# Kernel tuning notes

Measured on AMD Instinct MI355X. Metric: run time of the kernel, lower is better.

## Reference

```python
import jax, jax.numpy as jnp
import numpy as np

N = 16384   # 32 graphs x 512 nodes
E_RAND = 500000
H, C, D, F, L = 4, 64, 256, 1024, 4  # heads, head_dim, model dim, ffn dim, layers


def setup_inputs() -> dict:
    key = jax.random.key(0)
    ks = jax.random.split(key, 8)
    ei = jax.random.randint(ks[0], (2, E_RAND), 0, N)
    loops = jnp.arange(N)
    edge_index = jnp.concatenate([ei, jnp.stack([loops, loops])], axis=1)  # add_self_loops
    s = 0.05
    return dict(
        hf=jax.random.normal(ks[1], (N, D), dtype=jnp.float32),
        hs=jax.random.normal(ks[2], (N, D), dtype=jnp.float32),
        edge_index=edge_index,
        Wgat=jax.random.normal(ks[3], (2, L, D, D), dtype=jnp.float32) * s,
        att_src=jax.random.normal(ks[4], (2, L, H, C), dtype=jnp.float32) * s,
        att_dst=jax.random.normal(ks[5], (2, L, H, C), dtype=jnp.float32) * s,
        bias_gat=jnp.zeros((2, L, D), dtype=jnp.float32),
        W1=jax.random.normal(ks[6], (2, L, D, F), dtype=jnp.float32) * s,
        b1=jnp.zeros((2, L, F), dtype=jnp.float32),
        W2=jax.random.normal(ks[7], (2, L, F, D), dtype=jnp.float32) * s,
        b2=jnp.zeros((2, L, D), dtype=jnp.float32),
        g1=jnp.ones((2, L, D), dtype=jnp.float32),
        bt1=jnp.zeros((2, L, D), dtype=jnp.float32),
        g2=jnp.ones((2, L, D), dtype=jnp.float32),
        bt2=jnp.zeros((2, L, D), dtype=jnp.float32),
    )


def _ln(x, g, b):
    m = jnp.mean(x, -1, keepdims=True)
    v = jnp.var(x, -1, keepdims=True)
    return (x - m) * jax.lax.rsqrt(v + 1e-5) * g + b


def _gat_encoder_layer(x, src, dst, Wg, asr, ads, bg, W1, b1, W2, b2, g1, bt1, g2, bt2):
    # GATConv (PyG semantics): linear proj, per-edge attention, segment softmax over dst
    h = (x @ Wg).reshape(N, H, C)                       # [N,H,C]
    a_s = (h * asr).sum(-1)                             # [N,H]
    a_d = (h * ads).sum(-1)                             # [N,H]
    e = jax.nn.leaky_relu(a_s[src] + a_d[dst], 0.2)     # [E,H]
    m = jax.ops.segment_max(e, dst, num_segments=N)
    ex = jnp.exp(e - m[dst])
    den = jax.ops.segment_sum(ex, dst, num_segments=N)
    alpha = ex / jnp.maximum(den[dst], 1e-16)           # [E,H]
    agg = jax.ops.segment_sum(h[src] * alpha[:, :, None], dst, num_segments=N)
    out = agg.reshape(N, H * C) + bg                    # concat heads + bias
    # residual + norm1 (dropout=0.0)
    x1 = _ln(out + x, g1, bt1)
    # FFN + residual + norm2
    f = jax.nn.relu(x1 @ W1 + b1) @ W2 + b2
    return _ln(f + x1, g2, bt2)


def reference(hf, hs, edge_index, Wgat, att_src, att_dst, bias_gat, W1, b1, W2, b2, g1, bt1, g2, bt2):
    src, dst = edge_index[0], edge_index[1]
    for i in range(L):
        hf_new = _gat_encoder_layer(hf + hs, src, dst, Wgat[0, i], att_src[0, i], att_dst[0, i],
                                    bias_gat[0, i], W1[0, i], b1[0, i], W2[0, i], b2[0, i],
                                    g1[0, i], bt1[0, i], g2[0, i], bt2[0, i])
        hs = _gat_encoder_layer(hs, src, dst, Wgat[1, i], att_src[1, i], att_dst[1, i],
                                bias_gat[1, i], W1[1, i], b1[1, i], W2[1, i], b2[1, i],
                                g1[1, i], bt1[1, i], g2[1, i], bt2[1, i])
        hf = hf_new
    return (hf, hs)
```

## Files before the change

### kernel.cpp

```cpp
#include <hip/hip_runtime.h>

#define Nn 16384
#define Dm 256
#define Ff 1024

typedef __attribute__((ext_vector_type(8))) short bf16x8;
typedef __attribute__((ext_vector_type(4))) float f32x4;

typedef const __attribute__((address_space(1))) unsigned int glb_u32;
typedef __attribute__((address_space(3))) unsigned int lds_u32;

__device__ __forceinline__ void async_copy16(const void* g, void* l) {
  __builtin_amdgcn_global_load_lds((glb_u32*)g, (lds_u32*)l, 16, 0, 0);
}

__device__ __forceinline__ unsigned short f2bf(float f) {
  union { float f; unsigned u; } v; v.f = f;
  return (unsigned short)((v.u + 0x7FFFu + ((v.u >> 16) & 1u)) >> 16);
}

__device__ __forceinline__ float bf2f(unsigned short u) {
  union { unsigned u; float f; } v; v.u = ((unsigned)u) << 16;
  return v.f;
}

__device__ __forceinline__ float sel4(float4 v, int h) {
  float r = v.x;
  r = (h == 1) ? v.y : r;
  r = (h == 2) ? v.z : r;
  r = (h == 3) ? v.w : r;
  return r;
}

__global__ __launch_bounds__(256) void wconvt_kernel(const float* __restrict__ w,
                                                     unsigned short* __restrict__ wt,
                                                     int K, int J) {
  __shared__ unsigned short t[64][65];
  int b = blockIdx.z;
  int j0 = blockIdx.x * 64, k0 = blockIdx.y * 64;
  int tj = threadIdx.x & 63, q = threadIdx.x >> 6;
  const float* wb = w + (size_t)b * K * J;
#pragma unroll
  for (int r = 0; r < 16; ++r) {
    int k = r * 4 + q;
    t[k][tj] = f2bf(wb[(size_t)(k0 + k) * J + j0 + tj]);
  }
  __syncthreads();
  unsigned short* wtb = wt + (size_t)b * K * J;
#pragma unroll
  for (int r = 0; r < 16; ++r) {
    int j = r * 4 + q;
    wtb[(size_t)(j0 + j) * K + k0 + tj] = t[tj][j];
  }
}

__global__ void count_kernel(const int* __restrict__ dst, int E, int* __restrict__ cnt) {
  for (int e = blockIdx.x * blockDim.x + threadIdx.x; e < E; e += gridDim.x * blockDim.x)
    atomicAdd(&cnt[dst[e]], 1);
}

__global__ __launch_bounds__(256) void scan1_kernel(const int* __restrict__ cnt,
                                                    int* __restrict__ part,
                                                    int* __restrict__ bsum) {
  __shared__ int sd[256];
  int b = blockIdx.x, tid = threadIdx.x;
  int v = cnt[b * 256 + tid];
  sd[tid] = v;
  __syncthreads();
  for (int offt = 1; offt < 256; offt <<= 1) {
    int t = (tid >= offt) ? sd[tid - offt] : 0;
    __syncthreads();
    sd[tid] += t;
    __syncthreads();
  }
  part[b * 256 + tid] = sd[tid] - v;
  if (tid == 255) bsum[b] = sd[255];
}

__global__ __launch_bounds__(64) void scan2_kernel(const int* __restrict__ bsum,
                                                   int* __restrict__ bbase,
                                                   int* __restrict__ rowptr) {
  __shared__ int sd[64];
  int tid = threadIdx.x;
  int v = bsum[tid];
  sd[tid] = v;
  __syncthreads();
  for (int offt = 1; offt < 64; offt <<= 1) {
    int t = (tid >= offt) ? sd[tid - offt] : 0;
    __syncthreads();
    sd[tid] += t;
    __syncthreads();
  }
  bbase[tid] = sd[tid] - v;
  if (tid == 63) rowptr[Nn] = sd[63];
}

__global__ __launch_bounds__(256) void scan3_kernel(const int* __restrict__ part,
                                                    const int* __restrict__ bbase,
                                                    int* __restrict__ rowptr,
                                                    int* __restrict__ cursor) {
  int b = blockIdx.x, tid = threadIdx.x;
  int v = part[b * 256 + tid] + bbase[b];
  rowptr[b * 256 + tid] = v;
  cursor[b * 256 + tid] = v;
}

__global__ void fill_kernel(const int* __restrict__ src, const int* __restrict__ dst, int E,
                            int* __restrict__ cursor, int* __restrict__ csrc) {
  for (int e = blockIdx.x * blockDim.x + threadIdx.x; e < E; e += gridDim.x * blockDim.x) {
    int pos = atomicAdd(&cursor[dst[e]], 1);
    csrc[pos] = src[e];
  }
}

__global__ void prep_kernel(const float* __restrict__ hf, const float* __restrict__ hs,
                            float* __restrict__ x01f, unsigned short* __restrict__ x01b,
                            int total) {
  const size_t ZS = (size_t)Nn * Dm;
  for (int i = blockIdx.x * blockDim.x + threadIdx.x; i < total; i += gridDim.x * blockDim.x) {
    float a = hf[i], b = hs[i];
    float s = a + b;
    x01f[i] = s; x01b[i] = f2bf(s);
    x01f[ZS + i] = b; x01b[ZS + i] = f2bf(b);
  }
}

__global__ __launch_bounds__(256, 2) void proj_kernel(
    const unsigned short* __restrict__ xib, const unsigned short* __restrict__ Wgt_l,
    unsigned short* __restrict__ hbuf2, const float* __restrict__ asr_l,
    const float* __restrict__ ads_l, float* __restrict__ a_s2, float* __restrict__ a_d2) {
  __shared__ __align__(16) unsigned short sA[128 * 32];
  __shared__ __align__(16) unsigned short sB[64 * 32];
  const int K = 256;
  const size_t ZS = (size_t)Nn * Dm;
  int tid = threadIdx.x;
  int wave = tid >> 6, lane = tid & 63;
  int l16 = lane & 15, lhi = lane >> 4;
  int brow = blockIdx.x, bcol = blockIdx.y, z = blockIdx.z;
  int wm = wave >> 1, wn = wave & 1;

  const unsigned short* Ab = xib + z * ZS + (size_t)brow * 128 * K;
  const unsigned short* Bb = Wgt_l + (size_t)z * 4 * 65536 + (size_t)bcol * 64 * K;

  int ldrow = lane >> 2;
  int ldk = (lane & 3) * 8;

  f32x4 acc[4][2] = {};

  for (int k0 = 0; k0 < K; k0 += 32) {
    int r0 = wave * 16;
    async_copy16(Ab + (size_t)(r0 + ldrow) * K + k0 + ldk, &sA[r0 * 32]);
    async_copy16(Ab + (size_t)(r0 + 64 + ldrow) * K + k0 + ldk, &sA[(r0 + 64) * 32]);
    async_copy16(Bb + (size_t)(r0 + ldrow) * K + k0 + ldk, &sB[r0 * 32]);
    __syncthreads();
    bf16x8 af[4], bfr[2];
#pragma unroll
    for (int mi = 0; mi < 4; ++mi)
      af[mi] = *(const bf16x8*)&sA[(wm * 64 + mi * 16 + l16) * 32 + lhi * 8];
#pragma unroll
    for (int ni = 0; ni < 2; ++ni)
      bfr[ni] = *(const bf16x8*)&sB[(wn * 32 + ni * 16 + l16) * 32 + lhi * 8];
#pragma unroll
    for (int mi = 0; mi < 4; ++mi)
#pragma unroll
      for (int ni = 0; ni < 2; ++ni)
        acc[mi][ni] = __builtin_amdgcn_mfma_f32_16x16x32_bf16(af[mi], bfr[ni], acc[mi][ni], 0, 0, 0);
    __syncthreads();
  }

  unsigned short* hb = hbuf2 + z * ZS;
  const float* asr_p = asr_l + z * 1024 + bcol * 64;
  const float* ads_p = ads_l + z * 1024 + bcol * 64;
  float as0 = asr_p[wn * 32 + l16],      ad0 = ads_p[wn * 32 + l16];
  float as1 = asr_p[wn * 32 + 16 + l16], ad1 = ads_p[wn * 32 + 16 + l16];
  float* sredS = (float*)sA;
  float* sredD = (float*)sA + 256;

#pragma unroll
  for (int mi = 0; mi < 4; ++mi) {
#pragma unroll
    for (int j = 0; j < 4; ++j) {
      int r = brow * 128 + wm * 64 + mi * 16 + lhi * 4 + j;
      float v0 = acc[mi][0][j], v1 = acc[mi][1][j];
      hb[(size_t)r * 256 + bcol * 64 + wn * 32 + l16] = f2bf(v0);
      hb[(size_t)r * 256 + bcol * 64 + wn * 32 + 16 + l16] = f2bf(v1);
      float ps = v0 * as0 + v1 * as1;
      float pd = v0 * ad0 + v1 * ad1;
#pragma unroll
      for (int off = 1; off < 16; off <<= 1) {
        ps += __shfl_xor(ps, off);
        pd += __shfl_xor(pd, off);
      }
      if (l16 == 0) {
        int rl = mi * 16 + lhi * 4 + j;
        sredS[wm * 128 + wn * 64 + rl] = ps;
        sredD[wm * 128 + wn * 64 + rl] = pd;
      }
    }
  }
  __syncthreads();
  if (tid < 128) {
    int w = tid >> 6, rl = tid & 63;
    float s = sredS[w * 128 + rl] + sredS[w * 128 + 64 + rl];
    float d = sredD[w * 128 + rl] + sredD[w * 128 + 64 + rl];
    int row = brow * 128 + tid;
    a_s2[(size_t)z * Nn * 4 + row * 4 + bcol] = s;
    a_d2[(size_t)z * Nn * 4 + row * 4 + bcol] = d;
  }
}

__global__ __launch_bounds__(256, 2) void ffn1_kernel(
    const unsigned short* __restrict__ A2, const unsigned short* __restrict__ Bt_l,
    unsigned short* __restrict__ out2, const float* __restrict__ b1_l) {
  const int K = 256, Ncol = Ff;
  const size_t ZS = (size_t)Nn * Dm;
  __shared__ __align__(16) unsigned short sA[128 * 64];
  __shared__ __align__(16) unsigned short sB[128 * 64];
  int tid = threadIdx.x, wave = tid >> 6, lane = tid & 63;
  int l16 = lane & 15, lhi = lane >> 4;
  int brow = blockIdx.x, bcol = blockIdx.y, z = blockIdx.z;
  int wm = wave >> 1, wn = wave & 1;

  const unsigned short* Ab = A2 + z * ZS + (size_t)brow * 128 * K;
  const unsigned short* Bb = Bt_l + (size_t)z * 4 * Ff * 256 + (size_t)bcol * 128 * K;
  int lrow = lane >> 3, lk = (lane & 7) * 8;

  f32x4 acc[4][4] = {};

  for (int k0 = 0; k0 < K; k0 += 64) {
#pragma unroll
    for (int r = 0; r < 4; ++r) {
      int rb = r * 32 + wave * 8;
      async_copy16(Ab + (size_t)(rb + lrow) * K + k0 + lk, &sA[rb * 64]);
      async_copy16(Bb + (size_t)(rb + lrow) * K + k0 + lk, &sB[rb * 64]);
    }
    __syncthreads();
#pragma unroll
    for (int kk = 0; kk < 2; ++kk) {
      bf16x8 af[4], bfr[4];
#pragma unroll
      for (int mi = 0; mi < 4; ++mi)
        af[mi] = *(const bf16x8*)&sA[(wm * 64 + mi * 16 + l16) * 64 + kk * 32 + lhi * 8];
#pragma unroll
      for (int ni = 0; ni < 4; ++ni)
        bfr[ni] = *(const bf16x8*)&sB[(wn * 64 + ni * 16 + l16) * 64 + kk * 32 + lhi * 8];
#pragma unroll
      for (int mi = 0; mi < 4; ++mi)
#pragma unroll
        for (int ni = 0; ni < 4; ++ni)
          acc[mi][ni] = __builtin_amdgcn_mfma_f32_16x16x32_bf16(af[mi], bfr[ni], acc[mi][ni], 0, 0, 0);
    }
    __syncthreads();
  }

  unsigned short* outB = out2 + (size_t)z * Nn * Ff;
  const float* bias = b1_l + z * 4096;
#pragma unroll
  for (int mi = 0; mi < 4; ++mi) {
#pragma unroll
    for (int ni = 0; ni < 4; ++ni) {
#pragma unroll
      for (int j = 0; j < 4; ++j) {
        int r = brow * 128 + wm * 64 + mi * 16 + lhi * 4 + j;
        int c = bcol * 128 + wn * 64 + ni * 16 + l16;
        float v = acc[mi][ni][j] + bias[c];
        v = v > 0.f ? v : 0.f;
        outB[(size_t)r * Ncol + c] = f2bf(v);
      }
    }
  }
}

__global__ __launch_bounds__(256, 2) void ffn2_kernel(
    const unsigned short* __restrict__ A2, const unsigned short* __restrict__ Bt_l,
    float* __restrict__ out2, const float* __restrict__ b2_l,
    const float* __restrict__ resid2) {
  const int K = Ff, Ncol = 256;
  const size_t ZS = (size_t)Nn * Dm;
  __shared__ __align__(16) unsigned short sA[128 * 64];
  __shared__ __align__(16) unsigned short sB[64 * 64];
  int tid = threadIdx.x, wave = tid >> 6, lane = tid & 63;
  int l16 = lane & 15, lhi = lane >> 4;
  int brow = blockIdx.x, bcol = blockIdx.y, z = blockIdx.z;
  int wm = wave >> 1, wn = wave & 1;

  const unsigned short* Ab = A2 + (size_t)z * Nn * Ff + (size_t)brow * 128 * K;
  const unsigned short* Bb = Bt_l + (size_t)z * 4 * Ff * 256 + (size_t)bcol * 64 * K;
  int lrow = lane >> 3, lk = (lane & 7) * 8;

  f32x4 acc[4][2] = {};

  for (int k0 = 0; k0 < K; k0 += 64) {
#pragma unroll
    for (int r = 0; r < 4; ++r) {
      int rb = r * 32 + wave * 8;
      async_copy16(Ab + (size_t)(rb + lrow) * K + k0 + lk, &sA[rb * 64]);
      if (r < 2)
        async_copy16(Bb + (size_t)(rb + lrow) * K + k0 + lk, &sB[rb * 64]);
    }
    __syncthreads();
#pragma unroll
    for (int kk = 0; kk < 2; ++kk) {
      bf16x8 af[4], bfr[2];
#pragma unroll
      for (int mi = 0; mi < 4; ++mi)
        af[mi] = *(const bf16x8*)&sA[(wm * 64 + mi * 16 + l16) * 64 + kk * 32 + lhi * 8];
#pragma unroll
      for (int ni = 0; ni < 2; ++ni)
        bfr[ni] = *(const bf16x8*)&sB[(wn * 32 + ni * 16 + l16) * 64 + kk * 32 + lhi * 8];
#pragma unroll
      for (int mi = 0; mi < 4; ++mi)
#pragma unroll
        for (int ni = 0; ni < 2; ++ni)
          acc[mi][ni] = __builtin_amdgcn_mfma_f32_16x16x32_bf16(af[mi], bfr[ni], acc[mi][ni], 0, 0, 0);
    }
    __syncthreads();
  }

  float* outF = out2 + z * ZS;
  const float* bias = b2_l + z * 1024;
  const float* resid = resid2 + z * ZS;
#pragma unroll
  for (int mi = 0; mi < 4; ++mi) {
#pragma unroll
    for (int ni = 0; ni < 2; ++ni) {
#pragma unroll
      for (int j = 0; j < 4; ++j) {
        int r = brow * 128 + wm * 64 + mi * 16 + lhi * 4 + j;
        int c = bcol * 64 + wn * 32 + ni * 16 + l16;
        float v = acc[mi][ni][j] + bias[c] + resid[(size_t)r * Ncol + c];
        outF[(size_t)r * Ncol + c] = v;
      }
    }
  }
}

__global__ __launch_bounds__(256) void agg_kernel(
    const unsigned short* __restrict__ hbuf2, const float* __restrict__ a_s2,
    const float* __restrict__ a_d2,
    const int* __restrict__ rowptr, const int* __restrict__ csrc,
    const float* __restrict__ bias_l, const float* __restrict__ x01f,
    const float* __restrict__ g1_l, const float* __restrict__ bt1_l,
    float* __restrict__ x1f2, unsigned short* __restrict__ x1b2) {
  __shared__ float sw[4][320];
  __shared__ int ssrc[4][64];
  const size_t ZS = (size_t)Nn * Dm;
  int z = blockIdx.y;
  const unsigned short* hb = hbuf2 + z * ZS;
  const float* a_s = a_s2 + (size_t)z * Nn * 4;
  const float* a_d = a_d2 + (size_t)z * Nn * 4;
  const float* bias = bias_l + z * 1024;
  const float* xres = x01f + z * ZS;
  const float* g1 = g1_l + z * 1024;
  const float* bt1 = bt1_l + z * 1024;
  float* x1f = x1f2 + z * ZS;
  unsigned short* x1b = x1b2 + z * ZS;

  int wave = threadIdx.x >> 6, lane = threadIdx.x & 63;
  int n = blockIdx.x * 4 + wave;
  int l32 = lane & 31;
  int par = lane >> 5;
  int hch = l32 >> 3;
  int c0 = l32 * 8;
  int beg = rowptr[n], end = rowptr[n + 1];
  float4 adv = *(const float4*)&a_d[n * 4];
  const float NI = -__builtin_inff();
  float4 m4 = {NI, NI, NI, NI};
  float acc[8] = {};
  float den = 0.f;

  for (int base = beg; base < end; base += 64) {
    int cnt = min(64, end - base);
    float4 ev = {NI, NI, NI, NI};
    if (lane < cnt) {
      int s = csrc[base + lane];
      ssrc[wave][lane] = s;
      float4 as = *(const float4*)&a_s[s * 4];
      float e0 = as.x + adv.x; ev.x = e0 > 0.f ? e0 : 0.2f * e0;
      float e1 = as.y + adv.y; ev.y = e1 > 0.f ? e1 : 0.2f * e1;
      float e2 = as.z + adv.z; ev.z = e2 > 0.f ? e2 : 0.2f * e2;
      float e3 = as.w + adv.w; ev.w = e3 > 0.f ? e3 : 0.2f * e3;
    }
    float4 mv = ev;
#pragma unroll
    for (int off = 32; off; off >>= 1) {
      mv.x = fmaxf(mv.x, __shfl_xor(mv.x, off));
      mv.y = fmaxf(mv.y, __shfl_xor(mv.y, off));
      mv.z = fmaxf(mv.z, __shfl_xor(mv.z, off));
      mv.w = fmaxf(mv.w, __shfl_xor(mv.w, off));
    }
    float4 m4n;
    m4n.x = fmaxf(m4.x, mv.x); m4n.y = fmaxf(m4.y, mv.y);
    m4n.z = fmaxf(m4.z, mv.z); m4n.w = fmaxf(m4.w, mv.w);
    float rm = __expf(sel4(m4, hch) - sel4(m4n, hch));
#pragma unroll
    for (int j = 0; j < 8; ++j) acc[j] *= rm;
    den *= rm;
    if (lane < cnt) {
      float* swl = &sw[wave][lane * 5];
      swl[0] = __expf(ev.x - m4n.x);
      swl[1] = __expf(ev.y - m4n.y);
      swl[2] = __expf(ev.z - m4n.z);
      swl[3] = __expf(ev.w - m4n.w);
    }
    m4 = m4n;
    __builtin_amdgcn_wave_barrier();
    int i = par;
    for (; i + 2 < cnt; i += 4) {
      int s0 = ssrc[wave][i], s1 = ssrc[wave][i + 2];
      float w0 = sw[wave][i * 5 + hch], w1 = sw[wave][(i + 2) * 5 + hch];
      bf16x8 h0 = *(const bf16x8*)(hb + (size_t)s0 * 256 + c0);
      bf16x8 h1 = *(const bf16x8*)(hb + (size_t)s1 * 256 + c0);
#pragma unroll
      for (int j = 0; j < 8; ++j)
        acc[j] = fmaf(bf2f((unsigned short)h0[j]), w0, acc[j]);
#pragma unroll
      for (int j = 0; j < 8; ++j)
        acc[j] = fmaf(bf2f((unsigned short)h1[j]), w1, acc[j]);
      den += w0 + w1;
    }
    for (; i < cnt; i += 2) {
      float w = sw[wave][i * 5 + hch];
      int s_i = ssrc[wave][i];
      bf16x8 hv = *(const bf16x8*)(hb + (size_t)s_i * 256 + c0);
#pragma unroll
      for (int j = 0; j < 8; ++j)
        acc[j] = fmaf(bf2f((unsigned short)hv[j]), w, acc[j]);
      den += w;
    }
    __builtin_amdgcn_wave_barrier();
  }

#pragma unroll
  for (int j = 0; j < 8; ++j) acc[j] += __shfl_xor(acc[j], 32);
  den += __shfl_xor(den, 32);

  float invden = 1.f / fmaxf(den, 1e-16f);
  float outv[8];
  float s1 = 0.f, s2 = 0.f;
#pragma unroll
  for (int j = 0; j < 8; ++j) {
    float v = acc[j] * invden + bias[c0 + j] + xres[(size_t)n * 256 + c0 + j];
    outv[j] = v;
    s1 += v;
    s2 += v * v;
  }
#pragma unroll
  for (int off = 16; off; off >>= 1) {
    s1 += __shfl_xor(s1, off);
    s2 += __shfl_xor(s2, off);
  }
  float mean = s1 * (1.f / 256.f);
  float var = s2 * (1.f / 256.f) - mean * mean;
  float rst = rsqrtf(var + 1e-5f);
  if (par == 0) {
    float4 y0, y1;
    unsigned short yb[8];
#pragma unroll
    for (int j = 0; j < 8; ++j) {
      float y = (outv[j] - mean) * rst * g1[c0 + j] + bt1[c0 + j];
      if (j < 4) ((float*)&y0)[j] = y; else ((float*)&y1)[j - 4] = y;
      yb[j] = f2bf(y);
    }
    size_t idx = (size_t)n * 256 + c0;
    *(float4*)&x1f[idx] = y0;
    *(float4*)&x1f[idx + 4] = y1;
    *(bf16x8*)&x1b[idx] = *(bf16x8*)yb;
  }
}

template <int PREP>
__global__ __launch_bounds__(256) void ln2_kernel(const float* __restrict__ tf01,
                                                  const float* __restrict__ g2_l,
                                                  const float* __restrict__ bt2_l,
                                                  float* __restrict__ out_hf,
                                                  float* __restrict__ out_hs,
                                                  float* __restrict__ x01f,
                                                  unsigned short* __restrict__ x01b) {
  __shared__ float red[4][4];
  const size_t ZS = (size_t)Nn * Dm;
  int n = blockIdx.x, tid = threadIdx.x;
  int head = tid >> 6, lane = tid & 63;
  size_t idx = (size_t)n * 256 + tid;
  float v0 = tf01[idx], v1 = tf01[ZS + idx];
  float a0 = v0, b0 = v0 * v0, a1 = v1, b1 = v1 * v1;
#pragma unroll
  for (int off = 32; off; off >>= 1) {
    a0 += __shfl_xor(a0, off);
    b0 += __shfl_xor(b0, off);
    a1 += __shfl_xor(a1, off);
    b1 += __shfl_xor(b1, off);
  }
  if (lane == 0) { red[head][0] = a0; red[head][1] = b0; red[head][2] = a1; red[head][3] = b1; }
  __syncthreads();
  a0 = red[0][0] + red[1][0] + red[2][0] + red[3][0];
  b0 = red[0][1] + red[1][1] + red[2][1] + red[3][1];
  a1 = red[0][2] + red[1][2] + red[2][2] + red[3][2];
  b1 = red[0][3] + red[1][3] + red[2][3] + red[3][3];
  float m0 = a0 * (1.f / 256.f), m1 = a1 * (1.f / 256.f);
  float r0 = rsqrtf(b0 * (1.f / 256.f) - m0 * m0 + 1e-5f);
  float r1 = rsqrtf(b1 * (1.f / 256.f) - m1 * m1 + 1e-5f);
  float y0 = (v0 - m0) * r0 * g2_l[tid] + bt2_l[tid];
  float y1 = (v1 - m1) * r1 * g2_l[1024 + tid] + bt2_l[1024 + tid];
  out_hf[idx] = y0;
  out_hs[idx] = y1;
  if (PREP) {
    float s = y0 + y1;
    x01f[idx] = s;      x01b[idx] = f2bf(s);
    x01f[ZS + idx] = y1; x01b[ZS + idx] = f2bf(y1);
  }
}

extern "C" void kernel_launch(void* const* d_in, const int* in_sizes, int n_in,
                              void* d_out, int out_size, void* d_ws, size_t ws_size,
                              hipStream_t stream) {
  const float* hf_in = (const float*)d_in[0];
  const float* hs_in = (const float*)d_in[1];
  const int* ei = (const int*)d_in[2];
  const int E = in_sizes[2] / 2;
  const float* Wgat = (const float*)d_in[3];
  const float* att_src = (const float*)d_in[4];
  const float* att_dst = (const float*)d_in[5];
  const float* bias_gat = (const float*)d_in[6];
  const float* W1 = (const float*)d_in[7];
  const float* b1 = (const float*)d_in[8];
  const float* W2 = (const float*)d_in[9];
  const float* b2 = (const float*)d_in[10];
  const float* g1 = (const float*)d_in[11];
  const float* bt1 = (const float*)d_in[12];
  const float* g2 = (const float*)d_in[13];
  const float* bt2 = (const float*)d_in[14];
  const int* src = ei;
  const int* dst = ei + E;
  const size_t ZS = (size_t)Nn * Dm;

  char* wsp = (char*)d_ws;
  size_t off = 0;
  auto carve = [&](size_t bytes) -> void* {
    void* p = wsp + off;
    off += (bytes + 255) & ~(size_t)255;
    return p;
  };
  unsigned short* Wgt  = (unsigned short*)carve((size_t)8 * 256 * 256 * 2);
  unsigned short* W1t  = (unsigned short*)carve((size_t)8 * 256 * 1024 * 2);
  unsigned short* W2t  = (unsigned short*)carve((size_t)8 * 1024 * 256 * 2);
  int* cnt      = (int*)carve((size_t)Nn * 4);
  int* rowptr   = (int*)carve((size_t)(Nn + 1) * 4);
  int* cursor   = (int*)carve((size_t)Nn * 4);
  int* part     = (int*)carve((size_t)Nn * 4);
  int* bsum     = (int*)carve((size_t)64 * 4);
  int* bbase    = (int*)carve((size_t)64 * 4);
  int* csrc     = (int*)carve((size_t)E * 4);
  float* x01f   = (float*)carve(2 * ZS * 4);
  unsigned short* x01b = (unsigned short*)carve(2 * ZS * 2);
  unsigned short* hbuf2 = (unsigned short*)carve(2 * ZS * 2);
  float* a_s2   = (float*)carve((size_t)2 * Nn * 4 * 4);
  float* a_d2   = (float*)carve((size_t)2 * Nn * 4 * 4);
  float* x1f2   = (float*)carve(2 * ZS * 4);
  unsigned short* x1b2 = (unsigned short*)carve(2 * ZS * 2);
  unsigned short* f_b2 = (unsigned short*)carve((size_t)2 * Nn * Ff * 2);
  if (off > ws_size) return;

  wconvt_kernel<<<dim3(4, 4, 8), 256, 0, stream>>>(Wgat, Wgt, 256, 256);
  wconvt_kernel<<<dim3(16, 4, 8), 256, 0, stream>>>(W1, W1t, 256, 1024);
  wconvt_kernel<<<dim3(4, 16, 8), 256, 0, stream>>>(W2, W2t, 1024, 256);
  hipMemsetAsync(cnt, 0, (size_t)Nn * 4, stream);
  count_kernel<<<1024, 256, 0, stream>>>(dst, E, cnt);
  scan1_kernel<<<64, 256, 0, stream>>>(cnt, part, bsum);
  scan2_kernel<<<1, 64, 0, stream>>>(bsum, bbase, rowptr);
  scan3_kernel<<<64, 256, 0, stream>>>(part, bbase, rowptr, cursor);
  fill_kernel<<<1024, 256, 0, stream>>>(src, dst, E, cursor, csrc);

  float* out_hf = (float*)d_out;
  float* out_hs = out_hf + ZS;

  prep_kernel<<<2048, 256, 0, stream>>>(hf_in, hs_in, x01f, x01b, Nn * Dm);

  for (int l = 0; l < 4; ++l) {
    proj_kernel<<<dim3(128, 4, 2), 256, 0, stream>>>(
        x01b, Wgt + (size_t)l * 65536, hbuf2,
        att_src + l * 256, att_dst + l * 256, a_s2, a_d2);
    agg_kernel<<<dim3(Nn / 4, 2), 256, 0, stream>>>(
        hbuf2, a_s2, a_d2, rowptr, csrc,
        bias_gat + l * 256, x01f, g1 + l * 256, bt1 + l * 256, x1f2, x1b2);
    ffn1_kernel<<<dim3(128, 8, 2), 256, 0, stream>>>(
        x1b2, W1t + (size_t)l * 256 * 1024, f_b2, b1 + l * 1024);
    ffn2_kernel<<<dim3(128, 4, 2), 256, 0, stream>>>(
        f_b2, W2t + (size_t)l * 1024 * 256, x01f, b2 + l * 256, x1f2);
    if (l < 3) {
      ln2_kernel<1><<<Nn, 256, 0, stream>>>(x01f, g2 + l * 256, bt2 + l * 256,
                                            out_hf, out_hs, x01f, x01b);
    } else {
      ln2_kernel<0><<<Nn, 256, 0, stream>>>(x01f, g2 + l * 256, bt2 + l * 256,
                                            out_hf, out_hs, x01f, x01b);
    }
  }
}
```

Baseline: 769.2 us.

## Drop fp32 activation copies, use bf16 residuals, widen proj K-tile, restructure ln2

Removes the fp32 shadow buffers (x01f, x1f2) so residuals and the FFN output pass through bf16 only, which cuts global memory traffic in prep, agg, ffn2 and ln2. The proj GEMM moves from a K-tile of 32 to 64, halving the number of barrier-separated iterations. ln2 now handles one row per wave with vectorized loads instead of one row per block with an LDS reduction, and the agg inner loop loses its 2-way unrolled path. Residuals and pre-LN values are now rounded to bf16, which adds numerical error.

Result: faster. 659.0 us (-14.3%).

```diff
diff --git a/kernel.cpp b/kernel.cpp
--- a/kernel.cpp
+++ b/kernel.cpp
@@ -114,14 +114,12 @@
 }
 
 __global__ void prep_kernel(const float* __restrict__ hf, const float* __restrict__ hs,
-                            float* __restrict__ x01f, unsigned short* __restrict__ x01b,
-                            int total) {
+                            unsigned short* __restrict__ x01b, int total) {
   const size_t ZS = (size_t)Nn * Dm;
   for (int i = blockIdx.x * blockDim.x + threadIdx.x; i < total; i += gridDim.x * blockDim.x) {
     float a = hf[i], b = hs[i];
-    float s = a + b;
-    x01f[i] = s; x01b[i] = f2bf(s);
-    x01f[ZS + i] = b; x01b[ZS + i] = f2bf(b);
+    x01b[i] = f2bf(a + b);
+    x01b[ZS + i] = f2bf(b);
   }
 }
 
@@ -129,8 +127,8 @@
     const unsigned short* __restrict__ xib, const unsigned short* __restrict__ Wgt_l,
     unsigned short* __restrict__ hbuf2, const float* __restrict__ asr_l,
     const float* __restrict__ ads_l, float* __restrict__ a_s2, float* __restrict__ a_d2) {
-  __shared__ __align__(16) unsigned short sA[128 * 32];
-  __shared__ __align__(16) unsigned short sB[64 * 32];
+  __shared__ __align__(16) unsigned short sA[128 * 64];
+  __shared__ __align__(16) unsigned short sB[64 * 64];
   const int K = 256;
   const size_t ZS = (size_t)Nn * Dm;
   int tid = threadIdx.x;
@@ -141,30 +139,34 @@
 
   const unsigned short* Ab = xib + z * ZS + (size_t)brow * 128 * K;
   const unsigned short* Bb = Wgt_l + (size_t)z * 4 * 65536 + (size_t)bcol * 64 * K;
-
-  int ldrow = lane >> 2;
-  int ldk = (lane & 3) * 8;
+  int lrow = lane >> 3, lk = (lane & 7) * 8;
 
   f32x4 acc[4][2] = {};
 
-  for (int k0 = 0; k0 < K; k0 += 32) {
-    int r0 = wave * 16;
-    async_copy16(Ab + (size_t)(r0 + ldrow) * K + k0 + ldk, &sA[r0 * 32]);
-    async_copy16(Ab + (size_t)(r0 + 64 + ldrow) * K + k0 + ldk, &sA[(r0 + 64) * 32]);
-    async_copy16(Bb + (size_t)(r0 + ldrow) * K + k0 + ldk, &sB[r0 * 32]);
-    __syncthreads();
-    bf16x8 af[4], bfr[2];
-#pragma unroll
-    for (int mi = 0; mi < 4; ++mi)
-      af[mi] = *(const bf16x8*)&sA[(wm * 64 + mi * 16 + l16) * 32 + lhi * 8];
-#pragma unroll
-    for (int ni = 0; ni < 2; ++ni)
-      bfr[ni] = *(const bf16x8*)&sB[(wn * 32 + ni * 16 + l16) * 32 + lhi * 8];
-#pragma unroll
-    for (int mi = 0; mi < 4; ++mi)
+  for (int k0 = 0; k0 < K; k0 += 64) {
+#pragma unroll
+    for (int r = 0; r < 4; ++r) {
+      int rb = r * 32 + wave * 8;
+      async_copy16(Ab + (size_t)(rb + lrow) * K + k0 + lk, &sA[rb * 64]);
+      if (r < 2)
+        async_copy16(Bb + (size_t)(rb + lrow) * K + k0 + lk, &sB[rb * 64]);
+    }
+    __syncthreads();
+#pragma unroll
+    for (int kk = 0; kk < 2; ++kk) {
+      bf16x8 af[4], bfr[2];
+#pragma unroll
+      for (int mi = 0; mi < 4; ++mi)
+        af[mi] = *(const bf16x8*)&sA[(wm * 64 + mi * 16 + l16) * 64 + kk * 32 + lhi * 8];
 #pragma unroll
       for (int ni = 0; ni < 2; ++ni)
-        acc[mi][ni] = __builtin_amdgcn_mfma_f32_16x16x32_bf16(af[mi], bfr[ni], acc[mi][ni], 0, 0, 0);
+        bfr[ni] = *(const bf16x8*)&sB[(wn * 32 + ni * 16 + l16) * 64 + kk * 32 + lhi * 8];
+#pragma unroll
+      for (int mi = 0; mi < 4; ++mi)
+#pragma unroll
+        for (int ni = 0; ni < 2; ++ni)
+          acc[mi][ni] = __builtin_amdgcn_mfma_f32_16x16x32_bf16(af[mi], bfr[ni], acc[mi][ni], 0, 0, 0);
+    }
     __syncthreads();
   }
 
@@ -273,8 +275,8 @@
 
 __global__ __launch_bounds__(256, 2) void ffn2_kernel(
     const unsigned short* __restrict__ A2, const unsigned short* __restrict__ Bt_l,
-    float* __restrict__ out2, const float* __restrict__ b2_l,
-    const float* __restrict__ resid2) {
+    unsigned short* __restrict__ out2, const float* __restrict__ b2_l,
+    const unsigned short* __restrict__ resid2) {
   const int K = Ff, Ncol = 256;
   const size_t ZS = (size_t)Nn * Dm;
   __shared__ __align__(16) unsigned short sA[128 * 64];
@@ -317,9 +319,9 @@
     __syncthreads();
   }
 
-  float* outF = out2 + z * ZS;
+  unsigned short* outB = out2 + z * ZS;
   const float* bias = b2_l + z * 1024;
-  const float* resid = resid2 + z * ZS;
+  const unsigned short* resid = resid2 + z * ZS;
 #pragma unroll
   for (int mi = 0; mi < 4; ++mi) {
 #pragma unroll
@@ -328,8 +330,8 @@
       for (int j = 0; j < 4; ++j) {
         int r = brow * 128 + wm * 64 + mi * 16 + lhi * 4 + j;
         int c = bcol * 64 + wn * 32 + ni * 16 + l16;
-        float v = acc[mi][ni][j] + bias[c] + resid[(size_t)r * Ncol + c];
-        outF[(size_t)r * Ncol + c] = v;
+        float v = acc[mi][ni][j] + bias[c] + bf2f(resid[(size_t)r * Ncol + c]);
+        outB[(size_t)r * Ncol + c] = f2bf(v);
       }
     }
   }
@@ -339,9 +341,9 @@
     const unsigned short* __restrict__ hbuf2, const float* __restrict__ a_s2,
     const float* __restrict__ a_d2,
     const int* __restrict__ rowptr, const int* __restrict__ csrc,
-    const float* __restrict__ bias_l, const float* __restrict__ x01f,
+    const float* __restrict__ bias_l, const unsigned short* __restrict__ x01b,
     const float* __restrict__ g1_l, const float* __restrict__ bt1_l,
-    float* __restrict__ x1f2, unsigned short* __restrict__ x1b2) {
+    unsigned short* __restrict__ x1b2) {
   __shared__ float sw[4][320];
   __shared__ int ssrc[4][64];
   const size_t ZS = (size_t)Nn * Dm;
@@ -350,10 +352,9 @@
   const float* a_s = a_s2 + (size_t)z * Nn * 4;
   const float* a_d = a_d2 + (size_t)z * Nn * 4;
   const float* bias = bias_l + z * 1024;
-  const float* xres = x01f + z * ZS;
+  const unsigned short* xres = x01b + z * ZS;
   const float* g1 = g1_l + z * 1024;
   const float* bt1 = bt1_l + z * 1024;
-  float* x1f = x1f2 + z * ZS;
   unsigned short* x1b = x1b2 + z * ZS;
 
   int wave = threadIdx.x >> 6, lane = threadIdx.x & 63;
@@ -405,21 +406,7 @@
     }
     m4 = m4n;
     __builtin_amdgcn_wave_barrier();
-    int i = par;
-    for (; i + 2 < cnt; i += 4) {
-      int s0 = ssrc[wave][i], s1 = ssrc[wave][i + 2];
-      float w0 = sw[wave][i * 5 + hch], w1 = sw[wave][(i + 2) * 5 + hch];
-      bf16x8 h0 = *(const bf16x8*)(hb + (size_t)s0 * 256 + c0);
-      bf16x8 h1 = *(const bf16x8*)(hb + (size_t)s1 * 256 + c0);
-#pragma unroll
-      for (int j = 0; j < 8; ++j)
-        acc[j] = fmaf(bf2f((unsigned short)h0[j]), w0, acc[j]);
-#pragma unroll
-      for (int j = 0; j < 8; ++j)
-        acc[j] = fmaf(bf2f((unsigned short)h1[j]), w1, acc[j]);
-      den += w0 + w1;
-    }
-    for (; i < cnt; i += 2) {
+    for (int i = par; i < cnt; i += 2) {
       float w = sw[wave][i * 5 + hch];
       int s_i = ssrc[wave][i];
       bf16x8 hv = *(const bf16x8*)(hb + (size_t)s_i * 256 + c0);
@@ -436,11 +423,12 @@
   den += __shfl_xor(den, 32);
 
   float invden = 1.f / fmaxf(den, 1e-16f);
+  bf16x8 rv = *(const bf16x8*)(xres + (size_t)n * 256 + c0);
   float outv[8];
   float s1 = 0.f, s2 = 0.f;
 #pragma unroll
   for (int j = 0; j < 8; ++j) {
-    float v = acc[j] * invden + bias[c0 + j] + xres[(size_t)n * 256 + c0 + j];
+    float v = acc[j] * invden + bias[c0 + j] + bf2f((unsigned short)rv[j]);
     outv[j] = v;
     s1 += v;
     s2 += v * v;
@@ -454,36 +442,36 @@
   float var = s2 * (1.f / 256.f) - mean * mean;
   float rst = rsqrtf(var + 1e-5f);
   if (par == 0) {
-    float4 y0, y1;
     unsigned short yb[8];
 #pragma unroll
-    for (int j = 0; j < 8; ++j) {
-      float y = (outv[j] - mean) * rst * g1[c0 + j] + bt1[c0 + j];
-      if (j < 4) ((float*)&y0)[j] = y; else ((float*)&y1)[j - 4] = y;
-      yb[j] = f2bf(y);
-    }
-    size_t idx = (size_t)n * 256 + c0;
-    *(float4*)&x1f[idx] = y0;
-    *(float4*)&x1f[idx + 4] = y1;
-    *(bf16x8*)&x1b[idx] = *(bf16x8*)yb;
+    for (int j = 0; j < 8; ++j)
+      yb[j] = f2bf((outv[j] - mean) * rst * g1[c0 + j] + bt1[c0 + j]);
+    *(bf16x8*)&x1b[(size_t)n * 256 + c0] = *(bf16x8*)yb;
   }
 }
 
 template <int PREP>
-__global__ __launch_bounds__(256) void ln2_kernel(const float* __restrict__ tf01,
+__global__ __launch_bounds__(256) void ln2_kernel(const unsigned short* __restrict__ tb2,
                                                   const float* __restrict__ g2_l,
                                                   const float* __restrict__ bt2_l,
                                                   float* __restrict__ out_hf,
                                                   float* __restrict__ out_hs,
-                                                  float* __restrict__ x01f,
                                                   unsigned short* __restrict__ x01b) {
-  __shared__ float red[4][4];
-  const size_t ZS = (size_t)Nn * Dm;
-  int n = blockIdx.x, tid = threadIdx.x;
-  int head = tid >> 6, lane = tid & 63;
-  size_t idx = (size_t)n * 256 + tid;
-  float v0 = tf01[idx], v1 = tf01[ZS + idx];
-  float a0 = v0, b0 = v0 * v0, a1 = v1, b1 = v1 * v1;
+  const size_t ZS = (size_t)Nn * Dm;
+  int wave = threadIdx.x >> 6, lane = threadIdx.x & 63;
+  int n = blockIdx.x * 4 + wave;
+  int c0 = lane * 4;
+  size_t idx = (size_t)n * 256 + c0;
+  ushort4 u0 = *(const ushort4*)&tb2[idx];
+  ushort4 u1 = *(const ushort4*)&tb2[ZS + idx];
+  float v0[4] = {bf2f(u0.x), bf2f(u0.y), bf2f(u0.z), bf2f(u0.w)};
+  float v1[4] = {bf2f(u1.x), bf2f(u1.y), bf2f(u1.z), bf2f(u1.w)};
+  float a0 = 0.f, b0 = 0.f, a1 = 0.f, b1 = 0.f;
+#pragma unroll
+  for (int j = 0; j < 4; ++j) {
+    a0 += v0[j]; b0 += v0[j] * v0[j];
+    a1 += v1[j]; b1 += v1[j] * v1[j];
+  }
 #pragma unroll
   for (int off = 32; off; off >>= 1) {
     a0 += __shfl_xor(a0, off);
@@ -491,23 +479,24 @@
     a1 += __shfl_xor(a1, off);
     b1 += __shfl_xor(b1, off);
   }
-  if (lane == 0) { red[head][0] = a0; red[head][1] = b0; red[head][2] = a1; red[head][3] = b1; }
-  __syncthreads();
-  a0 = red[0][0] + red[1][0] + red[2][0] + red[3][0];
-  b0 = red[0][1] + red[1][1] + red[2][1] + red[3][1];
-  a1 = red[0][2] + red[1][2] + red[2][2] + red[3][2];
-  b1 = red[0][3] + red[1][3] + red[2][3] + red[3][3];
   float m0 = a0 * (1.f / 256.f), m1 = a1 * (1.f / 256.f);
   float r0 = rsqrtf(b0 * (1.f / 256.f) - m0 * m0 + 1e-5f);
   float r1 = rsqrtf(b1 * (1.f / 256.f) - m1 * m1 + 1e-5f);
-  float y0 = (v0 - m0) * r0 * g2_l[tid] + bt2_l[tid];
-  float y1 = (v1 - m1) * r1 * g2_l[1024 + tid] + bt2_l[1024 + tid];
-  out_hf[idx] = y0;
-  out_hs[idx] = y1;
+  float4 y0, y1;
+  unsigned short p0[4], p1[4];
+#pragma unroll
+  for (int j = 0; j < 4; ++j) {
+    float yf = (v0[j] - m0) * r0 * g2_l[c0 + j] + bt2_l[c0 + j];
+    float ys = (v1[j] - m1) * r1 * g2_l[1024 + c0 + j] + bt2_l[1024 + c0 + j];
+    ((float*)&y0)[j] = yf;
+    ((float*)&y1)[j] = ys;
+    if (PREP) { p0[j] = f2bf(yf + ys); p1[j] = f2bf(ys); }
+  }
+  *(float4*)&out_hf[idx] = y0;
+  *(float4*)&out_hs[idx] = y1;
   if (PREP) {
-    float s = y0 + y1;
-    x01f[idx] = s;      x01b[idx] = f2bf(s);
-    x01f[ZS + idx] = y1; x01b[ZS + idx] = f2bf(y1);
+    *(ushort4*)&x01b[idx] = *(ushort4*)p0;
+    *(ushort4*)&x01b[ZS + idx] = *(ushort4*)p1;
   }
 }
 
@@ -551,13 +540,12 @@
   int* bsum     = (int*)carve((size_t)64 * 4);
   int* bbase    = (int*)carve((size_t)64 * 4);
   int* csrc     = (int*)carve((size_t)E * 4);
-  float* x01f   = (float*)carve(2 * ZS * 4);
   unsigned short* x01b = (unsigned short*)carve(2 * ZS * 2);
   unsigned short* hbuf2 = (unsigned short*)carve(2 * ZS * 2);
   float* a_s2   = (float*)carve((size_t)2 * Nn * 4 * 4);
   float* a_d2   = (float*)carve((size_t)2 * Nn * 4 * 4);
-  float* x1f2   = (float*)carve(2 * ZS * 4);
   unsigned short* x1b2 = (unsigned short*)carve(2 * ZS * 2);
+  unsigned short* tb2  = (unsigned short*)carve(2 * ZS * 2);
   unsigned short* f_b2 = (unsigned short*)carve((size_t)2 * Nn * Ff * 2);
   if (off > ws_size) return;
 
@@ -574,7 +562,7 @@
   float* out_hf = (float*)d_out;
   float* out_hs = out_hf + ZS;
 
-  prep_kernel<<<2048, 256, 0, stream>>>(hf_in, hs_in, x01f, x01b, Nn * Dm);
+  prep_kernel<<<2048, 256, 0, stream>>>(hf_in, hs_in, x01b, Nn * Dm);
 
   for (int l = 0; l < 4; ++l) {
     proj_kernel<<<dim3(128, 4, 2), 256, 0, stream>>>(
@@ -582,17 +570,17 @@
         att_src + l * 256, att_dst + l * 256, a_s2, a_d2);
     agg_kernel<<<dim3(Nn / 4, 2), 256, 0, stream>>>(
         hbuf2, a_s2, a_d2, rowptr, csrc,
-        bias_gat + l * 256, x01f, g1 + l * 256, bt1 + l * 256, x1f2, x1b2);
+        bias_gat + l * 256, x01b, g1 + l * 256, bt1 + l * 256, x1b2);
     ffn1_kernel<<<dim3(128, 8, 2), 256, 0, stream>>>(
         x1b2, W1t + (size_t)l * 256 * 1024, f_b2, b1 + l * 1024);
     ffn2_kernel<<<dim3(128, 4, 2), 256, 0, stream>>>(
-        f_b2, W2t + (size_t)l * 1024 * 256, x01f, b2 + l * 256, x1f2);
+        f_b2, W2t + (size_t)l * 1024 * 256, tb2, b2 + l * 256, x1b2);
     if (l < 3) {
-      ln2_kernel<1><<<Nn, 256, 0, stream>>>(x01f, g2 + l * 256, bt2 + l * 256,
-                                            out_hf, out_hs, x01f, x01b);
+      ln2_kernel<1><<<Nn / 4, 256, 0, stream>>>(tb2, g2 + l * 256, bt2 + l * 256,
+                                                out_hf, out_hs, x01b);
     } else {
-      ln2_kernel<0><<<Nn, 256, 0, stream>>>(x01f, g2 + l * 256, bt2 + l * 256,
-                                            out_hf, out_hs, x01f, x01b);
-    }
-  }
-}
+      ln2_kernel<0><<<Nn / 4, 256, 0, stream>>>(tb2, g2 + l * 256, bt2 + l * 256,
+                                                out_hf, out_hs, x01b);
+    }
+  }
+}
```
